# Kernel tuning notes

Hardware: AMD Instinct MI355X
Metric: run time of the kernel (lower is better)

## Reference

```python
import jax, jax.numpy as jnp
import numpy as np

N, M, D = 32768, 2048, 512
TOPK = 10  # top 5 -> pseudo-normal, next 5 -> pseudo-abnormal


def setup_inputs() -> dict:
    key = jax.random.key(0)
    k1, k2 = jax.random.split(key)
    query = jax.random.normal(k1, (N, D), dtype=jnp.float32)
    m = jax.random.uniform(k2, (M, D), dtype=jnp.float32)
    m_items = m / jnp.linalg.norm(m, axis=1, keepdims=True)  # F.normalize dim=1
    return {"query": query, "m_items": m_items}


def reference(query, m_items):
    # scores over memory, softmax along memory dim (dim=1)
    score = query @ m_items.T                      # [N, M]
    score_memory = jax.nn.softmax(score, axis=1)    # [N, M]

    # top-10 per row (descending); first 5 = top, next 5 = bottom
    top10_scores, top10_idx = jax.lax.top_k(score_memory, TOPK)
    top_scores, bot_scores = top10_scores[:, :5], top10_scores[:, 5:10]
    top_idx, bot_idx = top10_idx[:, :5], top10_idx[:, 5:10]

    # softmax over selected subsets (temperature = 1)
    w_top = jax.nn.softmax(top_scores, axis=1)      # [N, 5]
    w_bot = jax.nn.softmax(bot_scores, axis=1)      # [N, 5]

    top_keys = m_items[top_idx]                     # [N, 5, D]
    bot_keys = m_items[bot_idx]                     # [N, 5, D]

    top_output = jnp.einsum('nk,nkd->nd', w_top, top_keys)
    bot_output = jnp.einsum('nk,nkd->nd', w_bot, bot_keys)

    pseudo_normal = 0.5 * query + 0.5 * top_output
    pseudo_abnormal = 0.01 * query + 0.99 * bot_output
    return (pseudo_normal, pseudo_abnormal)
```

## Files before the change

kernel.cpp:

```cpp
#include <hip/hip_runtime.h>
#include <hip/hip_bf16.h>

#define NQ 32768
#define MI 2048
#define DD 512

typedef unsigned int u32;
typedef unsigned short u16;
typedef unsigned long long u64;

typedef __attribute__((ext_vector_type(8))) short bf16x8;
typedef __attribute__((ext_vector_type(4))) float f32x4;


__device__ __forceinline__ u16 f2bf_rne(float f) {
  u32 u = __builtin_bit_cast(u32, f);
  u += 0x7FFFu + ((u >> 16) & 1u);
  return (u16)(u >> 16);
}

__device__ __forceinline__ u16 f2h(float f) {
  return __builtin_bit_cast(u16, (_Float16)f);
}

__device__ __forceinline__ float h2f(u16 h) {
  return (float)__builtin_bit_cast(_Float16, h);
}

__device__ __forceinline__ void gload16(const void* g, void* l) {
  const __attribute__((address_space(1))) u32* gp =
      (const __attribute__((address_space(1))) u32*)g;
  __attribute__((address_space(3))) u32* lp =
      (__attribute__((address_space(3))) u32*)(u32)(size_t)l;
  __builtin_amdgcn_global_load_lds(gp, lp, 16, 0, 0);
}


__global__ __launch_bounds__(256) void cvt_kernel(const float* __restrict__ in,
                                                  u16* __restrict__ out, int n8) {
  int stride = gridDim.x * blockDim.x;
  for (int i = blockIdx.x * blockDim.x + threadIdx.x; i < n8; i += stride) {
    const f32x4* p = (const f32x4*)in + (size_t)i * 2;
    f32x4 a = p[0], b = p[1];
    uint4 o;
    o.x = (u32)f2bf_rne(a[0]) | ((u32)f2bf_rne(a[1]) << 16);
    o.y = (u32)f2bf_rne(a[2]) | ((u32)f2bf_rne(a[3]) << 16);
    o.z = (u32)f2bf_rne(b[0]) | ((u32)f2bf_rne(b[1]) << 16);
    o.w = (u32)f2bf_rne(b[2]) | ((u32)f2bf_rne(b[3]) << 16);
    ((uint4*)out)[i] = o;
  }
}


__global__ __launch_bounds__(256) void gemm_kernel(const u16* __restrict__ Qb,
                                                   const u16* __restrict__ Mb,
                                                   u16* __restrict__ S) {
  __shared__ u16 As[128 * 64];
  __shared__ u16 Bs[128 * 64];
  const int t = threadIdx.x;
  const int l = t & 63, w = t >> 6;
  const int wr = w >> 1, wc = w & 1;
  const int bm = blockIdx.x >> 4, bn = blockIdx.x & 15;

  f32x4 acc[4][4] = {};
  const int l15 = l & 15, lg = l >> 4;

  const u16* Ag = Qb + (size_t)(bm * 128 + (t >> 3)) * DD + (t & 7) * 8;
  const u16* Bg = Mb + (size_t)(bn * 128 + (t >> 3)) * DD + (t & 7) * 8;
  char* Asl = (char*)As + t * 16;
  char* Bsl = (char*)Bs + t * 16;

  for (int kt = 0; kt < DD; kt += 64) {
#pragma unroll
    for (int i = 0; i < 4; ++i) {
      gload16(Ag + (size_t)i * 32 * DD + kt, Asl + i * 4096);
      gload16(Bg + (size_t)i * 32 * DD + kt, Bsl + i * 4096);
    }
    __syncthreads();
#pragma unroll
    for (int ks = 0; ks < 2; ++ks) {
      const int kk = ks * 32 + lg * 8;
      bf16x8 af[4], bfr[4];
#pragma unroll
      for (int mi = 0; mi < 4; ++mi)
        af[mi] = *(const bf16x8*)&As[(wr * 64 + mi * 16 + l15) * 64 + kk];
#pragma unroll
      for (int ni = 0; ni < 4; ++ni)
        bfr[ni] = *(const bf16x8*)&Bs[(wc * 64 + ni * 16 + l15) * 64 + kk];
#pragma unroll
      for (int mi = 0; mi < 4; ++mi)
#pragma unroll
        for (int ni = 0; ni < 4; ++ni)
          acc[mi][ni] = __builtin_amdgcn_mfma_f32_16x16x32_bf16(
              af[mi], bfr[ni], acc[mi][ni], 0, 0, 0);
    }
    __syncthreads();
  }

  const int r0 = bm * 128 + wr * 64 + (l >> 4) * 4;
  const int c0 = bn * 128 + wc * 64 + l15;
#pragma unroll
  for (int mi = 0; mi < 4; ++mi)
#pragma unroll
    for (int ni = 0; ni < 4; ++ni)
#pragma unroll
      for (int r = 0; r < 4; ++r)
        S[(size_t)(r0 + mi * 16 + r) * MI + (c0 + ni * 16)] = f2h(acc[mi][ni][r]);
}


__global__ __launch_bounds__(256) void finish_kernel(const float* __restrict__ q,
                                                     const float* __restrict__ m_items,
                                                     const u16* __restrict__ S,
                                                     float* __restrict__ out) {
  const int w = threadIdx.x >> 6, l = threadIdx.x & 63;
  const int n = blockIdx.x * 4 + w;

  const uint4* Sr = (const uint4*)(S + (size_t)n * MI);
  float v[32];
#pragma unroll
  for (int i = 0; i < 4; ++i) {
    uint4 c = Sr[i * 64 + l];
    v[i * 8 + 0] = h2f((u16)(c.x & 0xFFFF)); v[i * 8 + 1] = h2f((u16)(c.x >> 16));
    v[i * 8 + 2] = h2f((u16)(c.y & 0xFFFF)); v[i * 8 + 3] = h2f((u16)(c.y >> 16));
    v[i * 8 + 4] = h2f((u16)(c.z & 0xFFFF)); v[i * 8 + 5] = h2f((u16)(c.z >> 16));
    v[i * 8 + 6] = h2f((u16)(c.w & 0xFFFF)); v[i * 8 + 7] = h2f((u16)(c.w >> 16));
  }

  float mx = -1e30f;
#pragma unroll
  for (int j = 0; j < 32; ++j) mx = fmaxf(mx, v[j]);
  for (int off = 32; off >= 1; off >>= 1) mx = fmaxf(mx, __shfl_xor(mx, off));
  float se = 0.f;
#pragma unroll
  for (int j = 0; j < 32; ++j) se += __expf(v[j] - mx);
  for (int off = 32; off >= 1; off >>= 1) se += __shfl_xor(se, off);
  const float invZ = 1.0f / se;

  u32 u[32];
#pragma unroll
  for (int j = 0; j < 32; ++j) {
    u32 b = __builtin_bit_cast(u32, v[j]);
    b = (b & 0x80000000u) ? ~b : (b | 0x80000000u);
    u[j] = (b & ~31u) | (u32)(31 - j);
  }
  u32 pk = 0;
#pragma unroll
  for (int j = 0; j < 32; ++j) pk = pk > u[j] ? pk : u[j];

  int mym = 0x7FFFFFFF;
  float mysc = -1e30f;
  for (int c = 0; c < 16; ++c) {
    u32 g = pk;
    for (int off = 32; off >= 1; off >>= 1) {
      u32 o = __shfl_xor(g, off);
      g = g > o ? g : o;
    }
    u64 bal = __ballot(pk == g);
    int wl = (int)__ffsll(bal) - 1;
    int jw = 31 - (int)(g & 31u);
    int mwin = (jw >> 3) * 512 + wl * 8 + (jw & 7);
    if (l == c) mym = mwin;
    bool win = (l == wl);
#pragma unroll
    for (int j = 0; j < 32; ++j)
      if (j == jw && win) u[j] = 0u;
    pk = 0;
#pragma unroll
    for (int j = 0; j < 32; ++j) pk = pk > u[j] ? pk : u[j];
  }

  const f32x4* Q4 = (const f32x4*)(q + (size_t)n * DD);
  f32x4 q0 = Q4[l * 2], q1 = Q4[l * 2 + 1];
  for (int c = 0; c < 16; ++c) {
    int mc = __shfl(mym, c);
    const f32x4* M4 = (const f32x4*)(m_items + (size_t)mc * DD);
    f32x4 a = M4[l * 2], b = M4[l * 2 + 1];
    float p = a[0] * q0[0] + a[1] * q0[1] + a[2] * q0[2] + a[3] * q0[3] +
              b[0] * q1[0] + b[1] * q1[1] + b[2] * q1[2] + b[3] * q1[3];
    for (int off = 32; off >= 1; off >>= 1) p += __shfl_xor(p, off);
    if (l == c) mysc = p;
  }

  int rank = 0;
  for (int i = 0; i < 16; ++i) {
    float ov = __shfl(mysc, i);
    int om = __shfl(mym, i);
    rank += (ov > mysc || (ov == mysc && om < mym)) ? 1 : 0;
  }

  float prm = 0.f;
  int mr = 0;
  for (int r = 0; r < 10; ++r) {
    u64 bal = __ballot(rank == r);
    int sr = (int)__ffsll(bal) - 1;
    float sv = __shfl(mysc, sr);
    int sm = __shfl(mym, sr);
    float pv = __expf(sv - mx) * invZ;
    if (l == r) { prm = pv; mr = sm; }
  }

  f32x4 acc0a = q0 * 0.5f, acc0b = q1 * 0.5f;
  f32x4 acc1a = q0 * 0.01f, acc1b = q1 * 0.01f;

  float mt = -1e30f;
  for (int r = 0; r < 5; ++r) mt = fmaxf(mt, __shfl(prm, r));
  float Wt = 0.f;
  for (int r = 0; r < 5; ++r) Wt += __expf(__shfl(prm, r) - mt);
  float iWt = 0.5f / Wt;
  for (int r = 0; r < 5; ++r) {
    float pv = __shfl(prm, r);
    int mi = __shfl(mr, r);
    float wt = __expf(pv - mt) * iWt;
    const f32x4* M4 = (const f32x4*)(m_items + (size_t)mi * DD);
    acc0a += wt * M4[l * 2];
    acc0b += wt * M4[l * 2 + 1];
  }

  float mb = -1e30f;
  for (int r = 5; r < 10; ++r) mb = fmaxf(mb, __shfl(prm, r));
  float Wb = 0.f;
  for (int r = 5; r < 10; ++r) Wb += __expf(__shfl(prm, r) - mb);
  float iWb = 0.99f / Wb;
  for (int r = 5; r < 10; ++r) {
    float pv = __shfl(prm, r);
    int mi = __shfl(mr, r);
    float wt = __expf(pv - mb) * iWb;
    const f32x4* M4 = (const f32x4*)(m_items + (size_t)mi * DD);
    acc1a += wt * M4[l * 2];
    acc1b += wt * M4[l * 2 + 1];
  }

  f32x4* O0 = (f32x4*)(out + (size_t)n * DD);
  O0[l * 2] = acc0a;
  O0[l * 2 + 1] = acc0b;
  f32x4* O1 = (f32x4*)(out + (size_t)NQ * DD + (size_t)n * DD);
  O1[l * 2] = acc1a;
  O1[l * 2 + 1] = acc1b;
}


extern "C" void kernel_launch(void* const* d_in, const int* in_sizes, int n_in,
                              void* d_out, int out_size, void* d_ws, size_t ws_size,
                              hipStream_t stream) {
  const float* q = (const float*)d_in[0];
  const float* m = (const float*)d_in[1];
  float* out = (float*)d_out;

  u16* Qb = (u16*)d_ws;
  u16* Mb = Qb + (size_t)NQ * DD;
  u16* S = Mb + (size_t)MI * DD;

  cvt_kernel<<<2048, 256, 0, stream>>>(q, Qb, NQ * DD / 8);
  cvt_kernel<<<512, 256, 0, stream>>>(m, Mb, MI * DD / 8);
  gemm_kernel<<<(NQ / 128) * (MI / 128), 256, 0, stream>>>(Qb, Mb, S);
  finish_kernel<<<NQ / 4, 256, 0, stream>>>(q, m, S, out);
}
```

Before: 429.6 us.

## Pack score pairs into u32 stores, swizzle GEMM blocks, group-wise top-k selection

The GEMM epilogue now packs two adjacent rows' fp16 scores into one 32-bit word, so it issues half as many scattered 2-byte stores. The finish kernel reads the interleaved pairs and takes its row's half. Block indices are remapped so that blocks sharing an M-tile run across XCDs, which should improve L2 reuse. Top-k extraction now uses float keys with per-group-of-8 maxima, so each removal rescans only one group instead of all 32. The cost is that each finish wave reads twice the score bytes, since it fetches a row pair and discards half.

```diff
diff --git a/kernel.cpp b/kernel.cpp
--- a/kernel.cpp
+++ b/kernel.cpp
@@ -54,13 +54,15 @@
 
 __global__ __launch_bounds__(256) void gemm_kernel(const u16* __restrict__ Qb,
                                                    const u16* __restrict__ Mb,
-                                                   u16* __restrict__ S) {
+                                                   u32* __restrict__ SP) {
   __shared__ u16 As[128 * 64];
   __shared__ u16 Bs[128 * 64];
   const int t = threadIdx.x;
   const int l = t & 63, w = t >> 6;
   const int wr = w >> 1, wc = w & 1;
-  const int bm = blockIdx.x >> 4, bn = blockIdx.x & 15;
+  const int bid = blockIdx.x;
+  const int nb = (bid & 7) * 512 + (bid >> 3);
+  const int bm = nb >> 4, bn = nb & 15;
 
   f32x4 acc[4][4] = {};
   const int l15 = l & 15, lg = l >> 4;
@@ -99,75 +101,87 @@
 
   const int r0 = bm * 128 + wr * 64 + (l >> 4) * 4;
   const int c0 = bn * 128 + wc * 64 + l15;
+  const int p0 = r0 >> 1;
 #pragma unroll
   for (int mi = 0; mi < 4; ++mi)
 #pragma unroll
-    for (int ni = 0; ni < 4; ++ni)
-#pragma unroll
-      for (int r = 0; r < 4; ++r)
-        S[(size_t)(r0 + mi * 16 + r) * MI + (c0 + ni * 16)] = f2h(acc[mi][ni][r]);
-}
-
+    for (int ni = 0; ni < 4; ++ni) {
+      u32 lo = (u32)f2h(acc[mi][ni][0]) | ((u32)f2h(acc[mi][ni][1]) << 16);
+      u32 hi = (u32)f2h(acc[mi][ni][2]) | ((u32)f2h(acc[mi][ni][3]) << 16);
+      size_t base = (size_t)(p0 + mi * 8) * MI + (c0 + ni * 16);
+      SP[base] = lo;
+      SP[base + MI] = hi;
+    }
+}
+
+
+#define MAX8T(b) fmaxf(fmaxf(fmaxf(k[b], k[b + 1]), fmaxf(k[b + 2], k[b + 3])), \
+                       fmaxf(fmaxf(k[b + 4], k[b + 5]), fmaxf(k[b + 6], k[b + 7])))
+
+#define REMOVE_GRP(b, gvar)                                   \
+  {                                                           \
+    _Pragma("unroll") for (int j = 0; j < 8; ++j)             \
+        k[b + j] = (k[b + j] == gmax) ? -3e38f : k[b + j];    \
+    gvar = MAX8T(b);                                          \
+  }
 
 __global__ __launch_bounds__(256) void finish_kernel(const float* __restrict__ q,
                                                      const float* __restrict__ m_items,
-                                                     const u16* __restrict__ S,
+                                                     const u32* __restrict__ SP,
                                                      float* __restrict__ out) {
   const int w = threadIdx.x >> 6, l = threadIdx.x & 63;
   const int n = blockIdx.x * 4 + w;
-
-  const uint4* Sr = (const uint4*)(S + (size_t)n * MI);
-  float v[32];
-#pragma unroll
-  for (int i = 0; i < 4; ++i) {
+  const int p = n >> 1, h = n & 1;
+
+  const uint4* Sr = (const uint4*)(SP + (size_t)p * MI);
+  float k[32];
+#pragma unroll
+  for (int i = 0; i < 8; ++i) {
     uint4 c = Sr[i * 64 + l];
-    v[i * 8 + 0] = h2f((u16)(c.x & 0xFFFF)); v[i * 8 + 1] = h2f((u16)(c.x >> 16));
-    v[i * 8 + 2] = h2f((u16)(c.y & 0xFFFF)); v[i * 8 + 3] = h2f((u16)(c.y >> 16));
-    v[i * 8 + 4] = h2f((u16)(c.z & 0xFFFF)); v[i * 8 + 5] = h2f((u16)(c.z >> 16));
-    v[i * 8 + 6] = h2f((u16)(c.w & 0xFFFF)); v[i * 8 + 7] = h2f((u16)(c.w >> 16));
-  }
-
-  float mx = -1e30f;
-#pragma unroll
-  for (int j = 0; j < 32; ++j) mx = fmaxf(mx, v[j]);
+    u32 wd[4] = {c.x, c.y, c.z, c.w};
+#pragma unroll
+    for (int j = 0; j < 4; ++j) {
+      u16 hb = h ? (u16)(wd[j] >> 16) : (u16)(wd[j] & 0xFFFFu);
+      float f = h2f(hb);
+      int s = i * 4 + j;
+      k[s] = __builtin_bit_cast(float,
+                                (__builtin_bit_cast(u32, f) & ~31u) | (u32)(31 - s));
+    }
+  }
+
+  float mx = k[0];
+#pragma unroll
+  for (int j = 1; j < 32; ++j) mx = fmaxf(mx, k[j]);
   for (int off = 32; off >= 1; off >>= 1) mx = fmaxf(mx, __shfl_xor(mx, off));
   float se = 0.f;
 #pragma unroll
-  for (int j = 0; j < 32; ++j) se += __expf(v[j] - mx);
+  for (int j = 0; j < 32; ++j) se += __expf(k[j] - mx);
   for (int off = 32; off >= 1; off >>= 1) se += __shfl_xor(se, off);
   const float invZ = 1.0f / se;
 
-  u32 u[32];
-#pragma unroll
-  for (int j = 0; j < 32; ++j) {
-    u32 b = __builtin_bit_cast(u32, v[j]);
-    b = (b & 0x80000000u) ? ~b : (b | 0x80000000u);
-    u[j] = (b & ~31u) | (u32)(31 - j);
-  }
-  u32 pk = 0;
-#pragma unroll
-  for (int j = 0; j < 32; ++j) pk = pk > u[j] ? pk : u[j];
+  float g0 = MAX8T(0), g1 = MAX8T(8), g2 = MAX8T(16), g3 = MAX8T(24);
+  float pk = fmaxf(fmaxf(g0, g1), fmaxf(g2, g3));
 
   int mym = 0x7FFFFFFF;
   float mysc = -1e30f;
+#pragma unroll 1
   for (int c = 0; c < 16; ++c) {
-    u32 g = pk;
-    for (int off = 32; off >= 1; off >>= 1) {
-      u32 o = __shfl_xor(g, off);
-      g = g > o ? g : o;
-    }
-    u64 bal = __ballot(pk == g);
+    float gmax = pk;
+    for (int off = 32; off >= 1; off >>= 1) gmax = fmaxf(gmax, __shfl_xor(gmax, off));
+    u32 gb = __builtin_bit_cast(u32, gmax);
+    int jw = 31 - (int)(gb & 31u);
+    u64 bal = __ballot(pk == gmax);
     int wl = (int)__ffsll(bal) - 1;
-    int jw = 31 - (int)(g & 31u);
-    int mwin = (jw >> 3) * 512 + wl * 8 + (jw & 7);
+    int mwin = ((jw >> 2) << 8) + wl * 4 + (jw & 3);
     if (l == c) mym = mwin;
-    bool win = (l == wl);
-#pragma unroll
-    for (int j = 0; j < 32; ++j)
-      if (j == jw && win) u[j] = 0u;
-    pk = 0;
-#pragma unroll
-    for (int j = 0; j < 32; ++j) pk = pk > u[j] ? pk : u[j];
+    int grp = __builtin_amdgcn_readfirstlane(jw >> 3);
+    switch (grp) {
+      case 0: REMOVE_GRP(0, g0); break;
+      case 1: REMOVE_GRP(8, g1); break;
+      case 2: REMOVE_GRP(16, g2); break;
+      default: REMOVE_GRP(24, g3); break;
+    }
+    pk = fmaxf(fmaxf(g0, g1), fmaxf(g2, g3));
   }
 
   const f32x4* Q4 = (const f32x4*)(q + (size_t)n * DD);
@@ -176,10 +190,10 @@
     int mc = __shfl(mym, c);
     const f32x4* M4 = (const f32x4*)(m_items + (size_t)mc * DD);
     f32x4 a = M4[l * 2], b = M4[l * 2 + 1];
-    float p = a[0] * q0[0] + a[1] * q0[1] + a[2] * q0[2] + a[3] * q0[3] +
-              b[0] * q1[0] + b[1] * q1[1] + b[2] * q1[2] + b[3] * q1[3];
-    for (int off = 32; off >= 1; off >>= 1) p += __shfl_xor(p, off);
-    if (l == c) mysc = p;
+    float pr = a[0] * q0[0] + a[1] * q0[1] + a[2] * q0[2] + a[3] * q0[3] +
+               b[0] * q1[0] + b[1] * q1[1] + b[2] * q1[2] + b[3] * q1[3];
+    for (int off = 32; off >= 1; off >>= 1) pr += __shfl_xor(pr, off);
+    if (l == c) mysc = pr;
   }
 
   int rank = 0;
@@ -249,10 +263,10 @@
 
   u16* Qb = (u16*)d_ws;
   u16* Mb = Qb + (size_t)NQ * DD;
-  u16* S = Mb + (size_t)MI * DD;
+  u32* SP = (u32*)(Mb + (size_t)MI * DD);
 
   cvt_kernel<<<2048, 256, 0, stream>>>(q, Qb, NQ * DD / 8);
   cvt_kernel<<<512, 256, 0, stream>>>(m, Mb, MI * DD / 8);
-  gemm_kernel<<<(NQ / 128) * (MI / 128), 256, 0, stream>>>(Qb, Mb, S);
-  finish_kernel<<<NQ / 4, 256, 0, stream>>>(q, m, S, out);
-}
+  gemm_kernel<<<(NQ / 128) * (MI / 128), 256, 0, stream>>>(Qb, Mb, SP);
+  finish_kernel<<<NQ / 4, 256, 0, stream>>>(q, m, SP, out);
+}
```

Result: no change. 426.8 us (-0.6%).
